# Performance work log

Measured on AMD Instinct MI355X. Metric: run time of the kernel, lower is better.

## Reference

```python
import jax, jax.numpy as jnp
import numpy as np

B, DIN, H, DOUT = 4096, 2048, 4096, 2048


def setup_inputs() -> dict:
    key = jax.random.key(0)
    ks = jax.random.split(key, 17)
    x = jax.random.normal(ks[0], (B, DIN), dtype=jnp.float32)
    W0 = jax.random.randint(ks[1], (H, DIN), -127, 128, dtype=jnp.int32)
    b0 = jax.random.randint(ks[2], (H,), -127, 128, dtype=jnp.int32)
    W2 = jax.random.randint(ks[3], (H, H), -127, 128, dtype=jnp.int32)
    b2 = jax.random.randint(ks[4], (H,), -127, 128, dtype=jnp.int32)
    W4 = jax.random.randint(ks[5], (DOUT, H), -127, 128, dtype=jnp.int32)
    b4 = jax.random.randint(ks[6], (DOUT,), -127, 128, dtype=jnp.int32)
    # amax scalars: positive calibration ranges in [0.5, 2.0)
    amaxes = [jax.random.uniform(ks[7 + i], (), jnp.float32, 0.5, 2.0) for i in range(9)]
    (a0_in, a0_w, a0_b, a2_in, a2_w, a2_b, a4_in, a4_w, a4_b) = amaxes
    return {"x": x, "W0": W0, "b0": b0, "W2": W2, "b2": b2, "W4": W4, "b4": b4,
            "a0_in": a0_in, "a0_w": a0_w, "a0_b": a0_b,
            "a2_in": a2_in, "a2_w": a2_w, "a2_b": a2_b,
            "a4_in": a4_in, "a4_w": a4_w, "a4_b": a4_b}


def _quant(x, amax):
    # torch: clamp(round(x * 127/amax), -127, 127).int()
    scale = 127.0 / amax
    return jnp.clip(jnp.round(x * scale), -127.0, 127.0).astype(jnp.int32)


def _layer(x, W, b, a_in, a_w, a_b):
    xq = _quant(x, a_in)                                      # [B, in] int32
    acc = jnp.matmul(xq, W.T, preferred_element_type=jnp.int32)  # [B, out] int32
    y = acc.astype(jnp.float32) * (a_w * a_in / (127.0 ** 2))    # double dequant
    return y + b.astype(jnp.float32) * (a_b / 127.0)             # single dequant bias


def reference(x, W0, b0, W2, b2, W4, b4,
              a0_in, a0_w, a0_b, a2_in, a2_w, a2_b, a4_in, a4_w, a4_b):
    x = x.reshape(x.shape[0], -1)
    x = _layer(x, W0, b0, a0_in, a0_w, a0_b)
    x = jax.nn.relu(x)
    x = _layer(x, W2, b2, a2_in, a2_w, a2_b)
    x = jax.nn.relu(x)
    x = _layer(x, W4, b4, a4_in, a4_w, a4_b)
    return x
```

## Files before the change

kernel.cpp:

```cpp
#include <hip/hip_runtime.h>

using i32x4 = __attribute__((ext_vector_type(4))) int;

#define DEVI static __device__ __forceinline__

DEVI void gload_lds16(const void* g, void* l) {
  __builtin_amdgcn_global_load_lds(
      (const __attribute__((address_space(1))) void*)g,
      (__attribute__((address_space(3))) void*)l, 16, 0, 0);
}

template <int N> DEVI void vmcnt_n() {
  asm volatile("s_waitcnt vmcnt(%0)" ::"n"(N) : "memory");
}
template <int N> DEVI void lgkm_n() {
  asm volatile("s_waitcnt lgkmcnt(%0)" ::"n"(N) : "memory");
}

#define FENCE() asm volatile("" ::: "memory")
#define BARX()                    \
  do {                            \
    FENCE();                      \
    __builtin_amdgcn_s_barrier(); \
    FENCE();                      \
  } while (0)
#define SCHB() __builtin_amdgcn_sched_barrier(0)
#define PRIO1() __builtin_amdgcn_s_setprio(1)
#define PRIO0() __builtin_amdgcn_s_setprio(0)

DEVI int pack4(int4 v) {
  return (v.x & 255) | ((v.y & 255) << 8) | ((v.z & 255) << 16) | (v.w << 24);
}

DEVI int quant4(float4 v, float s) {
  float q;
  int r;
  q = fminf(fmaxf(rintf(__fmul_rn(v.x, s)), -127.0f), 127.0f);
  r = (int)q & 255;
  q = fminf(fmaxf(rintf(__fmul_rn(v.y, s)), -127.0f), 127.0f);
  r |= ((int)q & 255) << 8;
  q = fminf(fmaxf(rintf(__fmul_rn(v.z, s)), -127.0f), 127.0f);
  r |= ((int)q & 255) << 16;
  q = fminf(fmaxf(rintf(__fmul_rn(v.w, s)), -127.0f), 127.0f);
  r |= ((int)q & 255) << 24;
  return r;
}

__global__ void __launch_bounds__(256) prep_kernel(
    const int* __restrict__ W0, const int* __restrict__ W2,
    const int* __restrict__ W4, const float* __restrict__ x,
    const float* __restrict__ amax, signed char* __restrict__ W0q,
    signed char* __restrict__ W2q, signed char* __restrict__ W4q,
    signed char* __restrict__ xq, int n0, int n2, int n4, int nx,
    int s0, int s2, int s4, int sx) {
  const int bid = blockIdx.x;
  const int tid = threadIdx.x;
  if (bid < s0 + s2 + s4) {
    const int* w;
    signed char* o;
    int n, lb, nb;
    if (bid < s0) {
      w = W0; o = W0q; n = n0; lb = bid; nb = s0;
    } else if (bid < s0 + s2) {
      w = W2; o = W2q; n = n2; lb = bid - s0; nb = s2;
    } else {
      w = W4; o = W4q; n = n4; lb = bid - s0 - s2; nb = s4;
    }
    const int4* __restrict__ src = (const int4*)w;
    int* __restrict__ dst = (int*)o;
    const int T = nb * 256;
    int i = lb * 256 + tid;
    for (; i + 3 * T < n; i += 4 * T) {
      int4 a = src[i];
      int4 b = src[i + T];
      int4 c = src[i + 2 * T];
      int4 d = src[i + 3 * T];
      dst[i] = pack4(a);
      dst[i + T] = pack4(b);
      dst[i + 2 * T] = pack4(c);
      dst[i + 3 * T] = pack4(d);
    }
    for (; i < n; i += T) dst[i] = pack4(src[i]);
  } else {
    const float s = 127.0f / amax[0];
    const int lb = bid - s0 - s2 - s4;
    const float4* __restrict__ src = (const float4*)x;
    int* __restrict__ dst = (int*)xq;
    const int T = sx * 256;
    int i = lb * 256 + tid;
    for (; i + 3 * T < nx; i += 4 * T) {
      float4 a = src[i];
      float4 b = src[i + T];
      float4 c = src[i + 2 * T];
      float4 d = src[i + 3 * T];
      dst[i] = quant4(a, s);
      dst[i + T] = quant4(b, s);
      dst[i + 2 * T] = quant4(c, s);
      dst[i + 3 * T] = quant4(d, s);
    }
    for (; i < nx; i += T) dst[i] = quant4(src[i], s);
  }
}


#define STG(b, kt)                                                               \
  do {                                                                           \
    const int k0_ = (kt)*128 + scol;                                             \
    _Pragma("unroll") for (int j = 0; j < NN; ++j)                               \
        gload_lds16(Wb + (size_t)((j)*64 + srow) * K + k0_,                      \
                    &lds[b][ABYTES + (j)*8192 + tid * 16]);                      \
    gload_lds16(Ab + (size_t)(srow) * K + k0_, &lds[b][tid * 16]);               \
    gload_lds16(Ab + (size_t)(64 + srow) * K + k0_, &lds[b][8192 + tid * 16]);   \
    gload_lds16(Ab + (size_t)(128 + srow) * K + k0_, &lds[b][16384 + tid * 16]); \
    gload_lds16(Ab + (size_t)(192 + srow) * K + k0_, &lds[b][24576 + tid * 16]); \
  } while (0)

#define AF_(b, m, h) \
  (*(const i32x4*)&lds[b][(wrl + (m)*16 + ro) * 128 + ((h) ? cS1 : cS0)])
#define BF_(b, n, h) \
  (*(const i32x4*)&lds[b][ABYTES + (wcl + (n)*16 + ro) * 128 + ((h) ? cS1 : cS0)])

#define RD_AF(dst, b, m0)            \
  do {                               \
    dst[0][0] = AF_(b, m0, 0);       \
    dst[0][1] = AF_(b, m0, 1);       \
    dst[1][0] = AF_(b, (m0) + 1, 0); \
    dst[1][1] = AF_(b, (m0) + 1, 1); \
  } while (0)

#define READ_BF(b)                                   \
  do {                                               \
    _Pragma("unroll") for (int n = 0; n < NN; ++n) { \
      bf[n][0] = BF_(b, n, 0);                       \
      bf[n][1] = BF_(b, n, 1);                       \
    }                                                \
  } while (0)

#define MFMA_P(mp, af)                                                                     \
  do {                                                                                     \
    _Pragma("unroll") for (int n = 0; n < NN; ++n) {                                       \
      acc[2 * (mp)][n] =                                                                   \
          __builtin_amdgcn_mfma_i32_16x16x64_i8(af[0][0], bf[n][0], acc[2 * (mp)][n], 0, 0, 0); \
      acc[2 * (mp)][n] =                                                                   \
          __builtin_amdgcn_mfma_i32_16x16x64_i8(af[0][1], bf[n][1], acc[2 * (mp)][n], 0, 0, 0); \
      acc[2 * (mp) + 1][n] = __builtin_amdgcn_mfma_i32_16x16x64_i8(                        \
          af[1][0], bf[n][0], acc[2 * (mp) + 1][n], 0, 0, 0);                              \
      acc[2 * (mp) + 1][n] = __builtin_amdgcn_mfma_i32_16x16x64_i8(                        \
          af[1][1], bf[n][1], acc[2 * (mp) + 1][n], 0, 0, 0);                              \
    }                                                                                      \
  } while (0)

#define TILE_1B(b, t)                              \
  do {                                             \
    RD_AF(afX, b, 0);                              \
    READ_BF(b);                                    \
    RD_AF(afY, b, 2);                              \
    if ((t) + 1 < nt) STG(1 - (b), (t) + 1);       \
    lgkm_n<4>(); SCHB();                           \
    PRIO1(); MFMA_P(0, afX); PRIO0();              \
    RD_AF(afX, b, 4);                              \
    lgkm_n<4>(); SCHB();                           \
    PRIO1(); MFMA_P(1, afY); PRIO0();              \
    RD_AF(afY, b, 6);                              \
    lgkm_n<4>(); SCHB();                           \
    PRIO1(); MFMA_P(2, afX); PRIO0();              \
    lgkm_n<0>(); SCHB();                           \
    PRIO1(); MFMA_P(3, afY); PRIO0();              \
    vmcnt_n<0>();                                  \
  } while (0)

template <int BN, int OUT_I8>
__global__ __launch_bounds__(512, 2) void gemm_r17_kernel(
    const signed char* __restrict__ A, const signed char* __restrict__ W,
    const int* __restrict__ bias, void* __restrict__ out, int M, int N, int K,
    const float* __restrict__ p_ain, const float* __restrict__ p_aw,
    const float* __restrict__ p_ab, const float* __restrict__ p_anext) {
  static_assert(BN == 256 || BN == 128, "");
  constexpr int NN = BN / 64;
  constexpr int ABYTES = 256 * 128;
  __shared__ signed char lds[2][ABYTES + BN * 128];

  const int tid = threadIdx.x;
  const int lane = tid & 63;
  const int wave = tid >> 6;
  const int wrl = (wave >> 2) * 128;
  const int wcl = (wave & 3) * (BN / 4);

  const int lin = blockIdx.y * gridDim.x + blockIdx.x;
  const int cpx = (gridDim.x * gridDim.y) >> 3;
  const int swz = (lin & 7) * cpx + (lin >> 3);
  const int tileM = (swz / gridDim.x) * 256;
  const int tileN = (swz % gridDim.x) * BN;

  const signed char* Ab = A + (size_t)tileM * K;
  const signed char* Wb = W + (size_t)tileN * K;

  const int srow = tid >> 3;
  const int scol = ((tid & 7) ^ (srow & 7)) * 16;

  const int ro = lane & 15;
  const int kg = lane >> 4;
  const int cS0 = ((kg ^ (ro & 7)) << 4);
  const int cS1 = (((4 + kg) ^ (ro & 7)) << 4);

  const int nt = K >> 7;

  i32x4 acc[8][NN] = {};
  i32x4 afX[2][2], afY[2][2], bf[NN][2];

  STG(0, 0);
  vmcnt_n<0>();

  for (int t = 0; t < nt; t += 2) {
    BARX();
    TILE_1B(0, t);
    BARX();
    TILE_1B(1, t + 1);
  }

  const float s1 = __fmul_rn(p_aw[0], p_ain[0]) / 16129.0f;
  const float s2 = p_ab[0] / 127.0f;
  float qs = 0.0f;
  if (OUT_I8) qs = 127.0f / p_anext[0];

#pragma unroll
  for (int m = 0; m < 8; ++m) {
#pragma unroll
    for (int n = 0; n < NN; ++n) {
      const int col = tileN + wcl + n * 16 + ro;
      const int row0 = tileM + wrl + m * 16 + kg * 4;
      const float bv = __fmul_rn((float)bias[col], s2);
#pragma unroll
      for (int i = 0; i < 4; ++i) {
        float y = __fadd_rn(__fmul_rn((float)acc[m][n][i], s1), bv);
        if (OUT_I8) {
          float rl = fmaxf(y, 0.0f);
          float q = fminf(rintf(__fmul_rn(rl, qs)), 127.0f);
          ((signed char*)out)[(size_t)(row0 + i) * N + col] = (signed char)(int)q;
        } else {
          ((float*)out)[(size_t)(row0 + i) * N + col] = y;
        }
      }
    }
  }
}

extern "C" void kernel_launch(void* const* d_in, const int* in_sizes, int n_in,
                              void* d_out, int out_size, void* d_ws, size_t ws_size,
                              hipStream_t stream) {
  const float* x = (const float*)d_in[0];
  const int* W0 = (const int*)d_in[1];
  const int* b0 = (const int*)d_in[2];
  const int* W2 = (const int*)d_in[3];
  const int* b2 = (const int*)d_in[4];
  const int* W4 = (const int*)d_in[5];
  const int* b4 = (const int*)d_in[6];
  const float* a0_in = (const float*)d_in[7];
  const float* a0_w = (const float*)d_in[8];
  const float* a0_b = (const float*)d_in[9];
  const float* a2_in = (const float*)d_in[10];
  const float* a2_w = (const float*)d_in[11];
  const float* a2_b = (const float*)d_in[12];
  const float* a4_in = (const float*)d_in[13];
  const float* a4_w = (const float*)d_in[14];
  const float* a4_b = (const float*)d_in[15];

  constexpr int Bb = 4096, DIN = 2048, H = 4096, DOUT = 2048;
  constexpr size_t MB = 1u << 20;

  char* ws = (char*)d_ws;
  signed char* xq0 = (signed char*)(ws);
  signed char* xq2 = (signed char*)(ws);
  signed char* W0q = (signed char*)(ws + 8 * MB);
  signed char* W2q = (signed char*)(ws + 16 * MB);
  signed char* W4q = (signed char*)(ws + 32 * MB);
  signed char* xq1 = (signed char*)(ws + 40 * MB);

  const int n0 = H * DIN / 4, n2 = H * H / 4, n4 = DOUT * H / 4;
  const int nx = Bb * DIN / 4;
  const int s0 = 512, s2 = 1024, s4 = 512, sx = 512;
  prep_kernel<<<s0 + s2 + s4 + sx, 256, 0, stream>>>(
      W0, W2, W4, x, a0_in, W0q, W2q, W4q, xq0, n0, n2, n4, nx, s0, s2, s4, sx);

  gemm_r17_kernel<256, 1><<<dim3(H / 256, Bb / 256), 512, 0, stream>>>(
      xq0, W0q, b0, xq1, Bb, H, DIN, a0_in, a0_w, a0_b, a2_in);
  gemm_r17_kernel<256, 1><<<dim3(H / 256, Bb / 256), 512, 0, stream>>>(
      xq1, W2q, b2, xq2, Bb, H, H, a2_in, a2_w, a2_b, a4_in);
  gemm_r17_kernel<128, 0><<<dim3(DOUT / 128, Bb / 256), 512, 0, stream>>>(
      xq2, W4q, b4, d_out, Bb, DOUT, H, a4_in, a4_w, a4_b, a4_in);
}
```

Measured before the change: 159.0 us.

## Overlap next-layer weight int8 packing with current GEMM main loop

Takes the W2 and W4 int32-to-int8 packing out of the prep kernel and does it inside the GEMM of the preceding layer. Each block loads chunks of the next layer's weights into registers during its K loop and writes them packed one iteration later. The goal is to hide that memory-bound conversion behind MFMA work and make the prep kernel smaller. The cost is extra registers and global traffic inside the GEMM loop, which may reduce occupancy or disturb the tuned schedule.

```diff
diff --git a/kernel.cpp b/kernel.cpp
--- a/kernel.cpp
+++ b/kernel.cpp
@@ -47,30 +47,17 @@
 }
 
 __global__ void __launch_bounds__(256) prep_kernel(
-    const int* __restrict__ W0, const int* __restrict__ W2,
-    const int* __restrict__ W4, const float* __restrict__ x,
+    const int* __restrict__ W0, const float* __restrict__ x,
     const float* __restrict__ amax, signed char* __restrict__ W0q,
-    signed char* __restrict__ W2q, signed char* __restrict__ W4q,
-    signed char* __restrict__ xq, int n0, int n2, int n4, int nx,
-    int s0, int s2, int s4, int sx) {
+    signed char* __restrict__ xq, int n0, int nx, int s0, int sx) {
   const int bid = blockIdx.x;
   const int tid = threadIdx.x;
-  if (bid < s0 + s2 + s4) {
-    const int* w;
-    signed char* o;
-    int n, lb, nb;
-    if (bid < s0) {
-      w = W0; o = W0q; n = n0; lb = bid; nb = s0;
-    } else if (bid < s0 + s2) {
-      w = W2; o = W2q; n = n2; lb = bid - s0; nb = s2;
-    } else {
-      w = W4; o = W4q; n = n4; lb = bid - s0 - s2; nb = s4;
-    }
-    const int4* __restrict__ src = (const int4*)w;
-    int* __restrict__ dst = (int*)o;
-    const int T = nb * 256;
-    int i = lb * 256 + tid;
-    for (; i + 3 * T < n; i += 4 * T) {
+  if (bid < s0) {
+    const int4* __restrict__ src = (const int4*)W0;
+    int* __restrict__ dst = (int*)W0q;
+    const int T = s0 * 256;
+    int i = bid * 256 + tid;
+    for (; i + 3 * T < n0; i += 4 * T) {
       int4 a = src[i];
       int4 b = src[i + T];
       int4 c = src[i + 2 * T];
@@ -80,10 +67,10 @@
       dst[i + 2 * T] = pack4(c);
       dst[i + 3 * T] = pack4(d);
     }
-    for (; i < n; i += T) dst[i] = pack4(src[i]);
+    for (; i < n0; i += T) dst[i] = pack4(src[i]);
   } else {
     const float s = 127.0f / amax[0];
-    const int lb = bid - s0 - s2 - s4;
+    const int lb = bid - s0;
     const float4* __restrict__ src = (const float4*)x;
     int* __restrict__ dst = (int*)xq;
     const int T = sx * 256;
@@ -169,12 +156,13 @@
     vmcnt_n<0>();                                  \
   } while (0)
 
-template <int BN, int OUT_I8>
-__global__ __launch_bounds__(512, 2) void gemm_r17_kernel(
+template <int BN, int CPI, int OUT_I8>
+__global__ __launch_bounds__(512, 2) void gemm_r19_kernel(
     const signed char* __restrict__ A, const signed char* __restrict__ W,
     const int* __restrict__ bias, void* __restrict__ out, int M, int N, int K,
     const float* __restrict__ p_ain, const float* __restrict__ p_aw,
-    const float* __restrict__ p_ab, const float* __restrict__ p_anext) {
+    const float* __restrict__ p_ab, const float* __restrict__ p_anext,
+    const int* __restrict__ pw, signed char* __restrict__ po) {
   static_assert(BN == 256 || BN == 128, "");
   constexpr int NN = BN / 64;
   constexpr int ABYTES = 256 * 128;
@@ -207,15 +195,38 @@
 
   i32x4 acc[8][NN] = {};
   i32x4 afX[2][2], afY[2][2], bf[NN][2];
+  int4 wpk[CPI > 0 ? CPI : 1];
+  const size_t chunkbase = (size_t)lin * (CPI > 0 ? CPI * (nt >> 1) : 0);
 
   STG(0, 0);
   vmcnt_n<0>();
 
   for (int t = 0; t < nt; t += 2) {
+    if constexpr (CPI > 0) {
+      const int it = t >> 1;
+      if (it > 0) {
+#pragma unroll
+        for (int c = 0; c < CPI; ++c)
+          ((int*)po)[(chunkbase + (size_t)(it - 1) * CPI + c) * 512 + tid] =
+              pack4(wpk[c]);
+      }
+#pragma unroll
+      for (int c = 0; c < CPI; ++c)
+        wpk[c] =
+            *((const int4*)(pw + (chunkbase + (size_t)it * CPI + c) * 2048) +
+              tid);
+    }
     BARX();
     TILE_1B(0, t);
     BARX();
     TILE_1B(1, t + 1);
+  }
+  if constexpr (CPI > 0) {
+    const int itl = (nt >> 1) - 1;
+#pragma unroll
+    for (int c = 0; c < CPI; ++c)
+      ((int*)po)[(chunkbase + (size_t)itl * CPI + c) * 512 + tid] =
+          pack4(wpk[c]);
   }
 
   const float s1 = __fmul_rn(p_aw[0], p_ain[0]) / 16129.0f;
@@ -276,16 +287,15 @@
   signed char* W4q = (signed char*)(ws + 32 * MB);
   signed char* xq1 = (signed char*)(ws + 40 * MB);
 
-  const int n0 = H * DIN / 4, n2 = H * H / 4, n4 = DOUT * H / 4;
-  const int nx = Bb * DIN / 4;
-  const int s0 = 512, s2 = 1024, s4 = 512, sx = 512;
-  prep_kernel<<<s0 + s2 + s4 + sx, 256, 0, stream>>>(
-      W0, W2, W4, x, a0_in, W0q, W2q, W4q, xq0, n0, n2, n4, nx, s0, s2, s4, sx);
-
-  gemm_r17_kernel<256, 1><<<dim3(H / 256, Bb / 256), 512, 0, stream>>>(
-      xq0, W0q, b0, xq1, Bb, H, DIN, a0_in, a0_w, a0_b, a2_in);
-  gemm_r17_kernel<256, 1><<<dim3(H / 256, Bb / 256), 512, 0, stream>>>(
-      xq1, W2q, b2, xq2, Bb, H, H, a2_in, a2_w, a2_b, a4_in);
-  gemm_r17_kernel<128, 0><<<dim3(DOUT / 128, Bb / 256), 512, 0, stream>>>(
-      xq2, W4q, b4, d_out, Bb, DOUT, H, a4_in, a4_w, a4_b, a4_in);
-}
+  const int n0 = H * DIN / 4, nx = Bb * DIN / 4;
+  prep_kernel<<<2048, 256, 0, stream>>>(W0, x, a0_in, W0q, xq0, n0, nx, 1024,
+                                        1024);
+
+  gemm_r19_kernel<256, 4, 1><<<dim3(H / 256, Bb / 256), 512, 0, stream>>>(
+      xq0, W0q, b0, xq1, Bb, H, DIN, a0_in, a0_w, a0_b, a2_in, W2, W2q);
+  gemm_r19_kernel<256, 1, 1><<<dim3(H / 256, Bb / 256), 512, 0, stream>>>(
+      xq1, W2q, b2, xq2, Bb, H, H, a2_in, a2_w, a2_b, a4_in, W4, W4q);
+  gemm_r19_kernel<128, 0, 0><<<dim3(DOUT / 128, Bb / 256), 512, 0, stream>>>(
+      xq2, W4q, b4, d_out, Bb, DOUT, H, a4_in, a4_w, a4_b, a4_in, nullptr,
+      nullptr);
+}
```

After: 173.4 us. 1.09x slower.
